# Kernel tuning notes

Measured on AMD Instinct MI355X. Metric: run time of the kernel, lower is better.

## Reference

```python
import jax, jax.numpy as jnp
import numpy as np

GROUP = 32  # hadamard group size == MX block size


def _hadamard(n):
    H = np.array([[1.0]], dtype=np.float64)
    while H.shape[0] < n:
        H = np.block([[H, H], [H, -H]])
    return (H * n ** -0.5).astype(np.float32)


def _fp4_e2m1_rne(v):
    # round-to-nearest-even onto {0, 0.5, 1, 1.5, 2, 3, 4, 6} (signed)
    s = jnp.sign(v)
    a = jnp.minimum(jnp.abs(v), 6.0)
    e = jnp.clip(jnp.floor(jnp.log2(jnp.maximum(a, 2.0 ** -10))), 0.0, 2.0)
    step = jnp.exp2(e - 1.0)  # 0.5 / 1 / 2 depending on binade
    return s * jnp.round(a / step) * step  # jnp.round is half-to-even


def _mxfp4_quant_dequant(t):
    # blockwise MXFP4 with power-of-two (E8M0) shared scale per 32 elems
    shp = t.shape
    tb = t.reshape(-1, GROUP)
    amax = jnp.max(jnp.abs(tb), axis=-1, keepdims=True)
    # shared exponent: floor(log2(amax)) - emax_fp4 (=2, since max e2m1 = 6.0)
    scale = jnp.exp2(jnp.floor(jnp.log2(jnp.maximum(amax, 1e-30))) - 2.0)
    scale = jnp.where(amax > 0, scale, 1.0)
    return (_fp4_e2m1_rne(tb / scale) * scale).reshape(shp)


def _rotate(t, hadamard):
    g = hadamard.shape[0]
    return (t.reshape(-1, g) @ hadamard).reshape(t.shape)


def setup_inputs() -> dict:
    key = jax.random.key(0)
    k1, k2, k3 = jax.random.split(key, 3)
    tokens, in_f, out_f = 8192, 4096, 16384
    x = jax.random.normal(k1, (tokens, in_f), dtype=jnp.float32)
    weight = jax.random.normal(k2, (out_f, in_f), dtype=jnp.float32) * (in_f ** -0.5)
    bias = jax.random.normal(k3, (out_f,), dtype=jnp.float32) * 0.01
    hadamard = jnp.asarray(_hadamard(GROUP))
    return {"x": x, "weight": weight, "bias": bias, "hadamard": hadamard}


def reference(x, weight, bias, hadamard) -> jnp.ndarray:
    # pre_forward: dqweight = dequant(mxfp4_quant(hadamard_rotate(weight)))
    w_dq = _mxfp4_quant_dequant(_rotate(weight, hadamard))
    # forward: x -> hadamard rotate -> mxfp4 pseudoquant -> matmul -> +bias
    x_dq = _mxfp4_quant_dequant(_rotate(x, hadamard))
    return x_dq @ w_dq.T + bias
```

## Files before the change

kernel.cpp:

```cpp
#include <hip/hip_runtime.h>
#include <stdint.h>

typedef float v4f  __attribute__((ext_vector_type(4)));
typedef float v16f __attribute__((ext_vector_type(16)));
typedef int   v4i  __attribute__((ext_vector_type(4)));
typedef int   v8i  __attribute__((ext_vector_type(8)));

__device__ __forceinline__ void gload_lds16(const void* g, void* l) {
  __builtin_amdgcn_global_load_lds(
      (const __attribute__((address_space(1))) void*)g,
      (__attribute__((address_space(3))) void*)l, 16, 0, 0);
}
__device__ __forceinline__ void gload_lds4(const void* g, void* l) {
  __builtin_amdgcn_global_load_lds(
      (const __attribute__((address_space(1))) void*)g,
      (__attribute__((address_space(3))) void*)l, 4, 0, 0);
}

__global__ __launch_bounds__(256) void quant_fp4_kernel(
    const float* __restrict__ in, uint32_t* __restrict__ packed,
    uint8_t* __restrict__ scales, int R, int rshift) {
  int g = blockIdx.x * 256 + threadIdx.x;
  int kb = g >> rshift, row = g & (R - 1);

  float v[32];
  const v4f* p = (const v4f*)(in + (size_t)row * 4096 + kb * 32);
#pragma unroll
  for (int c = 0; c < 8; ++c) {
    v4f t = p[c];
    v[c * 4 + 0] = t[0]; v[c * 4 + 1] = t[1];
    v[c * 4 + 2] = t[2]; v[c * 4 + 3] = t[3];
  }
#pragma unroll
  for (int s = 0; s < 5; ++s) {
    const int h = 1 << s;
#pragma unroll
    for (int k = 0; k < 16; ++k) {
      const int i = ((k >> s) << (s + 1)) | (k & (h - 1));
      float a = v[i], b = v[i + h];
      v[i] = a + b; v[i + h] = a - b;
    }
  }
  const float RS = 0.17677669529663687f;
  float amax = 0.0f;
#pragma unroll
  for (int i = 0; i < 32; ++i) {
    v[i] *= RS;
    amax = fmaxf(amax, fabsf(v[i]));
  }
  int E;
  float rscale;
  if (amax > 0.0f) {
    float am = fmaxf(amax, 1e-30f);
    E = (int)((__float_as_uint(am) >> 23) & 255u) - 127;
    rscale = __uint_as_float((uint32_t)(2 - E + 127) << 23);
  } else { E = 2; rscale = 1.0f; }

  uint32_t dw[4] = {0u, 0u, 0u, 0u};
#pragma unroll
  for (int i = 0; i < 32; ++i) {
    float x = v[i];
    float a = fminf(fabsf(x) * rscale, 6.0f);
    float rstep = a >= 4.0f ? 0.5f : (a >= 2.0f ? 1.0f : 2.0f);
    float step  = a >= 4.0f ? 2.0f : (a >= 2.0f ? 1.0f : 0.5f);
    float q = rintf(a * rstep) * step;
    uint32_t uq = __float_as_uint(q);
    int Eq = (int)(uq >> 23) - 127;
    uint32_t code = (q == 0.0f) ? 0u
                  : (Eq < 0 ? 1u
                            : (((uint32_t)(Eq + 1) << 1) | ((uq >> 22) & 1u)));
    code |= (__float_as_uint(x) >> 31) << 3;
    dw[i >> 3] |= code << (4 * (i & 7));
  }
  uint4 o; o.x = dw[0]; o.y = dw[1]; o.z = dw[2]; o.w = dw[3];
  *(uint4*)(packed + (size_t)g * 4) = o;

  int kt = kb >> 3, hik = kb & 1, ks = (kb >> 1) & 3;
  scales[(size_t)((kt * 2 + hik) * R + row) * 4 + ks] = (uint8_t)(E - 2 + 127);
}

#define MFMA4(a, b, c, sa, sb) \
  __builtin_amdgcn_mfma_scale_f32_32x32x64_f8f6f4((a), (b), (c), 4, 4, 0, (sa), 0, (sb))
#define PAD8(x) __builtin_shufflevector((x), (x), 0, 1, 2, 3, -1, -1, -1, -1)
#define BARRIER { asm volatile("" ::: "memory"); __builtin_amdgcn_s_barrier(); asm volatile("" ::: "memory"); }
#define SB0 __builtin_amdgcn_sched_barrier(0)
#define LGKM(n) { asm volatile("s_waitcnt lgkmcnt(" #n ")" ::: "memory"); SB0; }
#define VMW(n)  asm volatile("s_waitcnt vmcnt(" #n ")" ::: "memory")

__global__ __launch_bounds__(512, 2) void gemm_fp4_8ph(
    const uint8_t* __restrict__ Apk, const uint8_t* __restrict__ Bpk,
    const uint32_t* __restrict__ Asc, const uint32_t* __restrict__ Bsc,
    const float* __restrict__ bias, float* __restrict__ C) {
  const int N = 16384;
  __shared__ uint8_t lds[139264];

  const int tid = threadIdx.x, lane = tid & 63, wv = tid >> 6;
  const int wm = wv >> 2, wn = wv & 3;
  const int hi = lane >> 5, r32 = lane & 31;

  const int bid = blockIdx.x;
  const int xcd = bid & 7, idx = bid >> 3, st = idx >> 5;
  const int mT = ((st & 3) * 8 + (idx & 7)) * 256;
  const int nT = (xcd * 8 + (st >> 2) * 4 + ((idx >> 3) & 3)) * 256;

  const int sOp = wv >> 2;
  const int sR2 = (wv >> 1) & 1;
  const int s0  = 2 * (wv & 1);
  const uint8_t* opBase = sOp ? Bpk : Apk;
  const size_t RB = sOp ? (size_t)16384 * 16 : (size_t)8192 * 16;
  const int T0 = sOp ? nT : mT;
  const size_t gOff0 = (size_t)(T0 + (s0 + 0) * 64 + lane) * 16;
  const size_t gOff1 = (size_t)(T0 + (s0 + 1) * 64 + lane) * 16;
  const int dOff0 = sOp * 32768 + sR2 * 4096 + (s0 + 0) * 1024 + lane * 16;
  const int dOff1 = sOp * 32768 + sR2 * 4096 + (s0 + 1) * 1024 + lane * 16;

  auto STG_OPS = [&](int kt, int a, int bb) {
    const uint8_t* g0 = opBase + (size_t)(kt * 8 + a + sR2) * RB;
    uint8_t* l = &lds[bb * 65536 + a * 4096];
    gload_lds16(g0 + gOff0, l + dOff0);
    gload_lds16(g0 + gOff1, l + dOff1);
  };

  const uint32_t* scBase = sOp ? Bsc : Asc;
  const int Rrows = sOp ? 16384 : 8192;
  auto STG_SC = [&](int kt, int bb) {
    const uint32_t* g = scBase + (size_t)(kt * 2 + sR2) * Rrows + T0;
    uint8_t* l = &lds[131072 + bb * 4096 + sOp * 2048 + sR2 * 1024];
    gload_lds4(g + (s0 + 0) * 64 + lane, l + (s0 + 0) * 256 + lane * 4);
    gload_lds4(g + (s0 + 1) * 64 + lane, l + (s0 + 1) * 256 + lane * 4);
  };

  const int aRd0 = hi * 4096 + (wm * 128 + r32) * 16;
  const int aRd1 = aRd0 + 65536;
  const int bRd0 = 32768 + hi * 4096 + (wn * 64 + r32) * 16;
  const int bRd1 = bRd0 + 65536;
  const int aSc0 = 131072 + hi * 1024 + (wm * 128 + r32) * 4;
  const int aSc1 = aSc0 + 4096;
  const int bSc0 = 131072 + 2048 + hi * 1024 + (wn * 64 + r32) * 4;
  const int bSc1 = bSc0 + 4096;

  v16f acc[4][2] = {};
  v4i fA0[4], fB0[2], fA1[4], fB1[2];
  uint32_t saD[4], sbD[2];

#define LDF(FA, FB, ARD, BRD, j) { \
    _Pragma("unroll") for (int mf = 0; mf < 4; ++mf) \
      FA[mf] = *(const v4i*)&lds[(ARD) + (j) * 8192 + mf * 512]; \
    _Pragma("unroll") for (int nf = 0; nf < 2; ++nf) \
      FB[nf] = *(const v4i*)&lds[(BRD) + (j) * 8192 + nf * 512]; }

#define SCRD(ASC, BSC) { \
    _Pragma("unroll") for (int mf = 0; mf < 4; ++mf) \
      saD[mf] = *(const uint32_t*)&lds[(ASC) + mf * 128]; \
    _Pragma("unroll") for (int nf = 0; nf < 2; ++nf) \
      sbD[nf] = *(const uint32_t*)&lds[(BSC) + nf * 128]; }

#define MM8(FA, FB, j) { \
    __builtin_amdgcn_s_setprio(1); \
    _Pragma("unroll") for (int mf = 0; mf < 4; ++mf) \
    _Pragma("unroll") for (int nf = 0; nf < 2; ++nf) \
      acc[mf][nf] = MFMA4(PAD8(FA[mf]), PAD8(FB[nf]), acc[mf][nf], \
                          (int)((saD[mf] >> (8 * (j))) & 255u), \
                          (int)((sbD[nf] >> (8 * (j))) & 255u)); \
    __builtin_amdgcn_s_setprio(0); }

#define TILE(bb, t, ARD, BRD, ASC, BSC, ob) { \
    SCRD(ASC, BSC); LDF(fA0, fB0, ARD, BRD, 0); SB0; LDF(fA1, fB1, ARD, BRD, 1); \
    STG_OPS((t) + 1, 6, ob); \
    BARRIER; LGKM(6); MM8(fA0, fB0, 0); BARRIER; \
    LDF(fA0, fB0, ARD, BRD, 2); \
    STG_OPS((t) + 2, 0, bb); STG_SC((t) + 2, bb); \
    BARRIER; LGKM(6); MM8(fA1, fB1, 1); BARRIER; \
    LDF(fA1, fB1, ARD, BRD, 3); \
    STG_OPS((t) + 2, 2, bb); \
    BARRIER; LGKM(6); MM8(fA0, fB0, 2); BARRIER; \
    STG_OPS((t) + 2, 4, bb); \
    BARRIER; LGKM(0); MM8(fA1, fB1, 3); \
    VMW(8); BARRIER; }

  STG_OPS(0, 0, 0); STG_OPS(0, 2, 0); STG_OPS(0, 4, 0); STG_OPS(0, 6, 0);
  STG_SC(0, 0);
  STG_OPS(1, 0, 1); STG_OPS(1, 2, 1); STG_OPS(1, 4, 1);
  STG_SC(1, 1);
  VMW(8);
  BARRIER;

#pragma unroll 1
  for (int i = 0; i < 7; ++i) {
    const int t0 = 2 * i;
    TILE(0, t0,     aRd0, bRd0, aSc0, bSc0, 1);
    TILE(1, t0 + 1, aRd1, bRd1, aSc1, bSc1, 0);
  }

  SCRD(aSc0, bSc0); LDF(fA0, fB0, aRd0, bRd0, 0); SB0; LDF(fA1, fB1, aRd0, bRd0, 1);
  STG_OPS(15, 6, 1);
  BARRIER; LGKM(6); MM8(fA0, fB0, 0); BARRIER;
  LDF(fA0, fB0, aRd0, bRd0, 2);
  BARRIER; LGKM(6); MM8(fA1, fB1, 1); BARRIER;
  LDF(fA1, fB1, aRd0, bRd0, 3);
  BARRIER; LGKM(6); MM8(fA0, fB0, 2); BARRIER;
  BARRIER; LGKM(0); MM8(fA1, fB1, 3);
  VMW(0); BARRIER;

  SCRD(aSc1, bSc1); LDF(fA0, fB0, aRd1, bRd1, 0); SB0; LDF(fA1, fB1, aRd1, bRd1, 1);
  BARRIER; LGKM(6); MM8(fA0, fB0, 0); BARRIER;
  LDF(fA0, fB0, aRd1, bRd1, 2);
  BARRIER; LGKM(6); MM8(fA1, fB1, 1); BARRIER;
  LDF(fA1, fB1, aRd1, bRd1, 3);
  BARRIER; LGKM(6); MM8(fA0, fB0, 2); BARRIER;
  BARRIER; LGKM(0); MM8(fA1, fB1, 3);

#pragma unroll
  for (int nf = 0; nf < 2; ++nf) {
    const int col = nT + wn * 64 + nf * 32 + r32;
    const float bv = bias[col];
#pragma unroll
    for (int mf = 0; mf < 4; ++mf) {
      const int rbase = mT + wm * 128 + mf * 32 + 4 * hi;
#pragma unroll
      for (int q = 0; q < 16; ++q) {
        const int rowl = (q & 3) + 8 * (q >> 2);
        C[(size_t)(rbase + rowl) * N + col] = acc[mf][nf][q] + bv;
      }
    }
  }
}

extern "C" void kernel_launch(void* const* d_in, const int* in_sizes, int n_in,
                              void* d_out, int out_size, void* d_ws, size_t ws_size,
                              hipStream_t stream) {
  const float* x    = (const float*)d_in[0];
  const float* w    = (const float*)d_in[1];
  const float* bias = (const float*)d_in[2];
  float* out = (float*)d_out;

  uint8_t* x_pk = (uint8_t*)d_ws;
  uint8_t* w_pk = x_pk + (size_t)16 * 1024 * 1024;
  uint8_t* x_sc = w_pk + (size_t)32 * 1024 * 1024;
  uint8_t* w_sc = x_sc + (size_t)1  * 1024 * 1024;

  quant_fp4_kernel<<<4096, 256, 0, stream>>>(x, (uint32_t*)x_pk, x_sc, 8192, 13);
  quant_fp4_kernel<<<8192, 256, 0, stream>>>(w, (uint32_t*)w_pk, w_sc, 16384, 14);

  gemm_fp4_8ph<<<2048, dim3(512), 0, stream>>>(
      x_pk, w_pk, (const uint32_t*)x_sc, (const uint32_t*)w_sc, bias, out);
}
```

Baseline: 486.6 us.

## Merge GEMM main-loop phases into two double-MFMA phases and retile quant blocks

The GEMM tile loop goes from four barrier-separated MFMA phases, each waiting on partial LDS counts, to two phases. Each phase issues two sets of fragment loads and two staging groups, waits with lgkmcnt(0), then runs two MFMA batches. This halves the number of barriers per tile and changes how many global loads stay outstanding (vmcnt 6 instead of 8), at the cost of less fine-grained overlap between LDS reads and MFMAs. The quant kernel now maps each block to an 8-row by 32-kblock patch so that global reads of the fp32 inputs are more localized, while the packed output keeps its kb-major layout.

```diff
diff --git a/kernel.cpp b/kernel.cpp
--- a/kernel.cpp
+++ b/kernel.cpp
@@ -19,9 +19,10 @@
 
 __global__ __launch_bounds__(256) void quant_fp4_kernel(
     const float* __restrict__ in, uint32_t* __restrict__ packed,
-    uint8_t* __restrict__ scales, int R, int rshift) {
-  int g = blockIdx.x * 256 + threadIdx.x;
-  int kb = g >> rshift, row = g & (R - 1);
+    uint8_t* __restrict__ scales, int R, int rblkbits) {
+  const int bid = blockIdx.x, tid = threadIdx.x;
+  const int row = ((bid & ((1 << rblkbits) - 1)) << 3) + (tid & 7);
+  const int kb  = ((bid >> rblkbits) << 5) + (tid >> 3);
 
   float v[32];
   const v4f* p = (const v4f*)(in + (size_t)row * 4096 + kb * 32);
@@ -73,9 +74,9 @@
     dw[i >> 3] |= code << (4 * (i & 7));
   }
   uint4 o; o.x = dw[0]; o.y = dw[1]; o.z = dw[2]; o.w = dw[3];
-  *(uint4*)(packed + (size_t)g * 4) = o;
-
-  int kt = kb >> 3, hik = kb & 1, ks = (kb >> 1) & 3;
+  *(uint4*)(packed + ((size_t)kb * R + row) * 4) = o;
+
+  const int kt = kb >> 3, hik = kb & 1, ks = (kb >> 1) & 3;
   scales[(size_t)((kt * 2 + hik) * R + row) * 4 + ks] = (uint8_t)(E - 2 + 127);
 }
 
@@ -84,10 +85,10 @@
 #define PAD8(x) __builtin_shufflevector((x), (x), 0, 1, 2, 3, -1, -1, -1, -1)
 #define BARRIER { asm volatile("" ::: "memory"); __builtin_amdgcn_s_barrier(); asm volatile("" ::: "memory"); }
 #define SB0 __builtin_amdgcn_sched_barrier(0)
-#define LGKM(n) { asm volatile("s_waitcnt lgkmcnt(" #n ")" ::: "memory"); SB0; }
+#define LGKM0 { asm volatile("s_waitcnt lgkmcnt(0)" ::: "memory"); SB0; }
 #define VMW(n)  asm volatile("s_waitcnt vmcnt(" #n ")" ::: "memory")
 
-__global__ __launch_bounds__(512, 2) void gemm_fp4_8ph(
+__global__ __launch_bounds__(512, 2) void gemm_fp4_2x(
     const uint8_t* __restrict__ Apk, const uint8_t* __restrict__ Bpk,
     const uint32_t* __restrict__ Asc, const uint32_t* __restrict__ Bsc,
     const float* __restrict__ bias, float* __restrict__ C) {
@@ -164,51 +165,53 @@
                           (int)((sbD[nf] >> (8 * (j))) & 255u)); \
     __builtin_amdgcn_s_setprio(0); }
 
-#define TILE(bb, t, ARD, BRD, ASC, BSC, ob) { \
-    SCRD(ASC, BSC); LDF(fA0, fB0, ARD, BRD, 0); SB0; LDF(fA1, fB1, ARD, BRD, 1); \
-    STG_OPS((t) + 1, 6, ob); \
-    BARRIER; LGKM(6); MM8(fA0, fB0, 0); BARRIER; \
-    LDF(fA0, fB0, ARD, BRD, 2); \
-    STG_OPS((t) + 2, 0, bb); STG_SC((t) + 2, bb); \
-    BARRIER; LGKM(6); MM8(fA1, fB1, 1); BARRIER; \
-    LDF(fA1, fB1, ARD, BRD, 3); \
-    STG_OPS((t) + 2, 2, bb); \
-    BARRIER; LGKM(6); MM8(fA0, fB0, 2); BARRIER; \
-    STG_OPS((t) + 2, 4, bb); \
-    BARRIER; LGKM(0); MM8(fA1, fB1, 3); \
-    VMW(8); BARRIER; }
+#define TILE2(bb, t, ARD, BRD, ASC, BSC, ob) { \
+     \
+    SCRD(ASC, BSC); \
+    LDF(fA0, fB0, ARD, BRD, 0); SB0; LDF(fA1, fB1, ARD, BRD, 1); \
+    STG_OPS((t) + 1, 4, ob); STG_OPS((t) + 1, 6, ob); SB0; \
+    BARRIER; LGKM0; \
+    MM8(fA0, fB0, 0); MM8(fA1, fB1, 1); \
+    BARRIER; \
+     \
+    LDF(fA0, fB0, ARD, BRD, 2); SB0; LDF(fA1, fB1, ARD, BRD, 3); \
+    STG_OPS((t) + 2, 0, bb); STG_OPS((t) + 2, 2, bb); STG_SC((t) + 2, bb); SB0; \
+    BARRIER; LGKM0; \
+    MM8(fA0, fB0, 2); MM8(fA1, fB1, 3); \
+    VMW(6); BARRIER; }
 
   STG_OPS(0, 0, 0); STG_OPS(0, 2, 0); STG_OPS(0, 4, 0); STG_OPS(0, 6, 0);
   STG_SC(0, 0);
-  STG_OPS(1, 0, 1); STG_OPS(1, 2, 1); STG_OPS(1, 4, 1);
+  STG_OPS(1, 0, 1); STG_OPS(1, 2, 1);
   STG_SC(1, 1);
-  VMW(8);
+  VMW(6);
   BARRIER;
 
 #pragma unroll 1
   for (int i = 0; i < 7; ++i) {
     const int t0 = 2 * i;
-    TILE(0, t0,     aRd0, bRd0, aSc0, bSc0, 1);
-    TILE(1, t0 + 1, aRd1, bRd1, aSc1, bSc1, 0);
-  }
-
-  SCRD(aSc0, bSc0); LDF(fA0, fB0, aRd0, bRd0, 0); SB0; LDF(fA1, fB1, aRd0, bRd0, 1);
-  STG_OPS(15, 6, 1);
-  BARRIER; LGKM(6); MM8(fA0, fB0, 0); BARRIER;
-  LDF(fA0, fB0, aRd0, bRd0, 2);
-  BARRIER; LGKM(6); MM8(fA1, fB1, 1); BARRIER;
-  LDF(fA1, fB1, aRd0, bRd0, 3);
-  BARRIER; LGKM(6); MM8(fA0, fB0, 2); BARRIER;
-  BARRIER; LGKM(0); MM8(fA1, fB1, 3);
+    TILE2(0, t0,     aRd0, bRd0, aSc0, bSc0, 1);
+    TILE2(1, t0 + 1, aRd1, bRd1, aSc1, bSc1, 0);
+  }
+
+  SCRD(aSc0, bSc0);
+  LDF(fA0, fB0, aRd0, bRd0, 0); SB0; LDF(fA1, fB1, aRd0, bRd0, 1);
+  STG_OPS(15, 4, 1); STG_OPS(15, 6, 1); SB0;
+  BARRIER; LGKM0;
+  MM8(fA0, fB0, 0); MM8(fA1, fB1, 1);
+  BARRIER;
+  LDF(fA0, fB0, aRd0, bRd0, 2); SB0; LDF(fA1, fB1, aRd0, bRd0, 3);
+  BARRIER; LGKM0;
+  MM8(fA0, fB0, 2); MM8(fA1, fB1, 3);
   VMW(0); BARRIER;
 
-  SCRD(aSc1, bSc1); LDF(fA0, fB0, aRd1, bRd1, 0); SB0; LDF(fA1, fB1, aRd1, bRd1, 1);
-  BARRIER; LGKM(6); MM8(fA0, fB0, 0); BARRIER;
-  LDF(fA0, fB0, aRd1, bRd1, 2);
-  BARRIER; LGKM(6); MM8(fA1, fB1, 1); BARRIER;
-  LDF(fA1, fB1, aRd1, bRd1, 3);
-  BARRIER; LGKM(6); MM8(fA0, fB0, 2); BARRIER;
-  BARRIER; LGKM(0); MM8(fA1, fB1, 3);
+  SCRD(aSc1, bSc1);
+  LDF(fA0, fB0, aRd1, bRd1, 0); SB0; LDF(fA1, fB1, aRd1, bRd1, 1);
+  LGKM0;
+  MM8(fA0, fB0, 0); MM8(fA1, fB1, 1);
+  LDF(fA0, fB0, aRd1, bRd1, 2); SB0; LDF(fA1, fB1, aRd1, bRd1, 3);
+  LGKM0;
+  MM8(fA0, fB0, 2); MM8(fA1, fB1, 3);
 
 #pragma unroll
   for (int nf = 0; nf < 2; ++nf) {
@@ -239,9 +242,9 @@
   uint8_t* x_sc = w_pk + (size_t)32 * 1024 * 1024;
   uint8_t* w_sc = x_sc + (size_t)1  * 1024 * 1024;
 
-  quant_fp4_kernel<<<4096, 256, 0, stream>>>(x, (uint32_t*)x_pk, x_sc, 8192, 13);
-  quant_fp4_kernel<<<8192, 256, 0, stream>>>(w, (uint32_t*)w_pk, w_sc, 16384, 14);
-
-  gemm_fp4_8ph<<<2048, dim3(512), 0, stream>>>(
+  quant_fp4_kernel<<<4096, 256, 0, stream>>>(x, (uint32_t*)x_pk, x_sc, 8192, 10);
+  quant_fp4_kernel<<<8192, 256, 0, stream>>>(w, (uint32_t*)w_pk, w_sc, 16384, 11);
+
+  gemm_fp4_2x<<<2048, dim3(512), 0, stream>>>(
       x_pk, w_pk, (const uint32_t*)x_sc, (const uint32_t*)w_sc, bias, out);
 }
```

Result: faster. 453.4 us (-6.8%).
